# Kernel tuning notes

Measured on AMD Instinct MI355X. Metric: run time of the kernel, lower is better.

Reference implementation:

```python
import jax, jax.numpy as jnp
import numpy as np

EPS = 1e-8

def setup_inputs() -> dict:
    key = jax.random.key(0)
    k1, k2, k3 = jax.random.split(key, 3)
    B, D, H, W = 32, 96, 96, 96
    x = jax.random.normal(k1, (B, 1, D, H, W), dtype=jnp.float32)
    mask = jax.random.randint(k2, (1, 1, D, H, W), 0, 2, dtype=jnp.int32)
    weight = jax.random.normal(k3, (2, 1, D, H, W), dtype=jnp.float32) * 0.01
    bias = jnp.zeros((2,), dtype=jnp.float32)
    return {"x": x, "mask": mask, "weight": weight, "bias": bias}

def reference(x, mask, weight, bias):
    # effective positions: |x| > eps AND mask nonzero (values are NOT scaled by mask)
    gate = (jnp.abs(x) > EPS) & (mask != 0)          # (B,1,D,H,W) via broadcast
    xg = jnp.where(gate, x, jnp.zeros((), x.dtype))  # masked input
    # per-batch sparse dot products == dense masked contraction over all spatial dims
    out = jnp.einsum('bidhw,cidhw->bc', xg, weight) + bias  # (B, 2)
    # original reshapes to (B,2,1,1,1) then Flatten -> (B,2)
    return out
```

## Files before the change

kernel.cpp:

```cpp
#include <hip/hip_runtime.h>
#include <hip/hip_bf16.h>

#define EPS 1e-8f

constexpr int B_ = 32;
constexpr int N_ = 96 * 96 * 96;
constexpr int N4 = N_ / 4;
constexpr int TPB = 256;
constexpr int BPW = 8;
constexpr int NBLK = 1024;

__global__ __launch_bounds__(TPB) void partial_kernel(
    const float4* __restrict__ x,
    const int4*   __restrict__ mask,
    const float4* __restrict__ w,
    float*        __restrict__ partials)
{
    const int tid  = threadIdx.x;
    const int wave = tid >> 6;
    const int lane = tid & 63;
    const int b0   = wave * BPW;

    float acc[BPW][2];
#pragma unroll
    for (int bb = 0; bb < BPW; ++bb) { acc[bb][0] = 0.f; acc[bb][1] = 0.f; }

    const int stride = gridDim.x * 64;
    for (int i4 = blockIdx.x * 64 + lane; i4 < N4; i4 += stride) {
        const int4   mi = mask[i4];
        const float4 w0 = w[i4];
        const float4 w1 = w[N4 + i4];
        const float m0 = mi.x ? 1.f : 0.f;
        const float m1 = mi.y ? 1.f : 0.f;
        const float m2 = mi.z ? 1.f : 0.f;
        const float m3 = mi.w ? 1.f : 0.f;
        const float wm0x = w0.x * m0, wm0y = w0.y * m1, wm0z = w0.z * m2, wm0w = w0.w * m3;
        const float wm1x = w1.x * m0, wm1y = w1.y * m1, wm1z = w1.z * m2, wm1w = w1.w * m3;

#pragma unroll
        for (int bb = 0; bb < BPW; ++bb) {
            const float4 xv = x[(size_t)(b0 + bb) * N4 + i4];
            const float g0 = (fabsf(xv.x) > EPS) ? xv.x : 0.f;
            const float g1 = (fabsf(xv.y) > EPS) ? xv.y : 0.f;
            const float g2 = (fabsf(xv.z) > EPS) ? xv.z : 0.f;
            const float g3 = (fabsf(xv.w) > EPS) ? xv.w : 0.f;
            float a0 = acc[bb][0], a1 = acc[bb][1];
            a0 = fmaf(g0, wm0x, a0); a0 = fmaf(g1, wm0y, a0);
            a0 = fmaf(g2, wm0z, a0); a0 = fmaf(g3, wm0w, a0);
            a1 = fmaf(g0, wm1x, a1); a1 = fmaf(g1, wm1y, a1);
            a1 = fmaf(g2, wm1z, a1); a1 = fmaf(g3, wm1w, a1);
            acc[bb][0] = a0; acc[bb][1] = a1;
        }
    }

#pragma unroll
    for (int bb = 0; bb < BPW; ++bb) {
#pragma unroll
        for (int c = 0; c < 2; ++c) {
            float v = acc[bb][c];
            v += __shfl_xor(v, 32, 64);
            v += __shfl_xor(v, 16, 64);
            v += __shfl_xor(v,  8, 64);
            v += __shfl_xor(v,  4, 64);
            v += __shfl_xor(v,  2, 64);
            v += __shfl_xor(v,  1, 64);
            acc[bb][c] = v;
        }
    }

    __shared__ float lds[64];
    if (lane == 0) {
#pragma unroll
        for (int bb = 0; bb < BPW; ++bb) {
            lds[(b0 + bb) * 2 + 0] = acc[bb][0];
            lds[(b0 + bb) * 2 + 1] = acc[bb][1];
        }
    }
    __syncthreads();
    if (tid < 64) partials[(size_t)tid * gridDim.x + blockIdx.x] = lds[tid];
}

__global__ __launch_bounds__(256) void finalize_kernel(
    const float4* __restrict__ partials4,
    const float*  __restrict__ bias,
    float* __restrict__ out, int nblk4)
{
    const int j    = blockIdx.x;
    const int tid  = threadIdx.x;
    const int wave = tid >> 6;
    const int lane = tid & 63;

    float s = 0.f;
    for (int k = tid; k < nblk4; k += 256) {
        const float4 v = partials4[(size_t)j * nblk4 + k];
        s += (v.x + v.y) + (v.z + v.w);
    }
    s += __shfl_xor(s, 32, 64);
    s += __shfl_xor(s, 16, 64);
    s += __shfl_xor(s,  8, 64);
    s += __shfl_xor(s,  4, 64);
    s += __shfl_xor(s,  2, 64);
    s += __shfl_xor(s,  1, 64);

    __shared__ float red[4];
    if (lane == 0) red[wave] = s;
    __syncthreads();
    if (tid == 0)
        out[j] = (red[0] + red[1]) + (red[2] + red[3]) + bias[j & 1];
}

extern "C" void kernel_launch(void* const* d_in, const int* in_sizes, int n_in,
                              void* d_out, int out_size, void* d_ws, size_t ws_size,
                              hipStream_t stream) {
    const float4* x    = (const float4*)d_in[0];
    const int4*   mask = (const int4*)d_in[1];
    const float4* w    = (const float4*)d_in[2];
    const float*  bias = (const float*)d_in[3];
    float* out = (float*)d_out;
    float* partials = (float*)d_ws;

    int nblk = NBLK;
    const size_t need = (size_t)nblk * 64 * sizeof(float);
    if (ws_size < need) {
        nblk = (int)(ws_size / (64 * sizeof(float)));
        if (nblk < 4) nblk = 4;
        nblk &= ~3;
    }

    partial_kernel<<<nblk, TPB, 0, stream>>>(x, mask, w, partials);
    finalize_kernel<<<64, 256, 0, stream>>>((const float4*)partials, bias, out,
                                            nblk / 4);
}
```

Baseline: 29.02 us.

## Fully unroll grid-stride loop with double-buffered register prefetch

Adds a specialized kernel for the fixed 1024-block grid. The grid-stride loop (3–4 iterations per lane) is fully unrolled with two register stages, so the loads for the next iteration are issued before the current one is computed, giving more memory requests in flight. Each wave's lane 0 now writes partials straight to global memory instead of staging them through LDS behind a block barrier. This raises register pressure (two stages of 11 float4 each) and could reduce occupancy.

```diff
diff --git a/kernel.cpp b/kernel.cpp
--- a/kernel.cpp
+++ b/kernel.cpp
@@ -1,58 +1,59 @@
 #include <hip/hip_runtime.h>
-#include <hip/hip_bf16.h>
 
 #define EPS 1e-8f
 
-constexpr int B_ = 32;
-constexpr int N_ = 96 * 96 * 96;
-constexpr int N4 = N_ / 4;
-constexpr int TPB = 256;
-constexpr int BPW = 8;
+constexpr int N4   = 221184;
+constexpr int TPB  = 256;
+constexpr int BPW  = 8;
 constexpr int NBLK = 1024;
+constexpr int STR  = NBLK * 64;
 
-__global__ __launch_bounds__(TPB) void partial_kernel(
-    const float4* __restrict__ x,
-    const int4*   __restrict__ mask,
-    const float4* __restrict__ w,
-    float*        __restrict__ partials)
+struct Stage {
+    int4   mi;
+    float4 w0, w1;
+    float4 xv[BPW];
+};
+
+__device__ __forceinline__ void load_stage(Stage& s,
+        const float4* __restrict__ x, const int4* __restrict__ mask,
+        const float4* __restrict__ w, int i4, int b0)
 {
-    const int tid  = threadIdx.x;
-    const int wave = tid >> 6;
-    const int lane = tid & 63;
-    const int b0   = wave * BPW;
+    s.mi = mask[i4];
+    s.w0 = w[i4];
+    s.w1 = w[N4 + i4];
+#pragma unroll
+    for (int bb = 0; bb < BPW; ++bb)
+        s.xv[bb] = x[(size_t)(b0 + bb) * N4 + i4];
+}
 
-    float acc[BPW][2];
+__device__ __forceinline__ void compute_stage(const Stage& s, float (&acc)[BPW][2])
+{
+    const float m0 = s.mi.x ? 1.f : 0.f;
+    const float m1 = s.mi.y ? 1.f : 0.f;
+    const float m2 = s.mi.z ? 1.f : 0.f;
+    const float m3 = s.mi.w ? 1.f : 0.f;
+    const float wm0x = s.w0.x * m0, wm0y = s.w0.y * m1, wm0z = s.w0.z * m2, wm0w = s.w0.w * m3;
+    const float wm1x = s.w1.x * m0, wm1y = s.w1.y * m1, wm1z = s.w1.z * m2, wm1w = s.w1.w * m3;
 #pragma unroll
-    for (int bb = 0; bb < BPW; ++bb) { acc[bb][0] = 0.f; acc[bb][1] = 0.f; }
+    for (int bb = 0; bb < BPW; ++bb) {
+        const float4 xv = s.xv[bb];
+        const float g0 = (fabsf(xv.x) > EPS) ? xv.x : 0.f;
+        const float g1 = (fabsf(xv.y) > EPS) ? xv.y : 0.f;
+        const float g2 = (fabsf(xv.z) > EPS) ? xv.z : 0.f;
+        const float g3 = (fabsf(xv.w) > EPS) ? xv.w : 0.f;
+        float a0 = acc[bb][0], a1 = acc[bb][1];
+        a0 = fmaf(g0, wm0x, a0); a0 = fmaf(g1, wm0y, a0);
+        a0 = fmaf(g2, wm0z, a0); a0 = fmaf(g3, wm0w, a0);
+        a1 = fmaf(g0, wm1x, a1); a1 = fmaf(g1, wm1y, a1);
+        a1 = fmaf(g2, wm1z, a1); a1 = fmaf(g3, wm1w, a1);
+        acc[bb][0] = a0; acc[bb][1] = a1;
+    }
+}
 
-    const int stride = gridDim.x * 64;
-    for (int i4 = blockIdx.x * 64 + lane; i4 < N4; i4 += stride) {
-        const int4   mi = mask[i4];
-        const float4 w0 = w[i4];
-        const float4 w1 = w[N4 + i4];
-        const float m0 = mi.x ? 1.f : 0.f;
-        const float m1 = mi.y ? 1.f : 0.f;
-        const float m2 = mi.z ? 1.f : 0.f;
-        const float m3 = mi.w ? 1.f : 0.f;
-        const float wm0x = w0.x * m0, wm0y = w0.y * m1, wm0z = w0.z * m2, wm0w = w0.w * m3;
-        const float wm1x = w1.x * m0, wm1y = w1.y * m1, wm1z = w1.z * m2, wm1w = w1.w * m3;
-
-#pragma unroll
-        for (int bb = 0; bb < BPW; ++bb) {
-            const float4 xv = x[(size_t)(b0 + bb) * N4 + i4];
-            const float g0 = (fabsf(xv.x) > EPS) ? xv.x : 0.f;
-            const float g1 = (fabsf(xv.y) > EPS) ? xv.y : 0.f;
-            const float g2 = (fabsf(xv.z) > EPS) ? xv.z : 0.f;
-            const float g3 = (fabsf(xv.w) > EPS) ? xv.w : 0.f;
-            float a0 = acc[bb][0], a1 = acc[bb][1];
-            a0 = fmaf(g0, wm0x, a0); a0 = fmaf(g1, wm0y, a0);
-            a0 = fmaf(g2, wm0z, a0); a0 = fmaf(g3, wm0w, a0);
-            a1 = fmaf(g0, wm1x, a1); a1 = fmaf(g1, wm1y, a1);
-            a1 = fmaf(g2, wm1z, a1); a1 = fmaf(g3, wm1w, a1);
-            acc[bb][0] = a0; acc[bb][1] = a1;
-        }
-    }
-
+__device__ __forceinline__ void reduce_and_store(
+        float (&acc)[BPW][2], int wave, int lane, int b0, int bid, int nblk,
+        float* __restrict__ partials)
+{
 #pragma unroll
     for (int bb = 0; bb < BPW; ++bb) {
 #pragma unroll
@@ -67,22 +68,71 @@
             acc[bb][c] = v;
         }
     }
-
-    __shared__ float lds[64];
     if (lane == 0) {
 #pragma unroll
         for (int bb = 0; bb < BPW; ++bb) {
-            lds[(b0 + bb) * 2 + 0] = acc[bb][0];
-            lds[(b0 + bb) * 2 + 1] = acc[bb][1];
+            partials[(size_t)((b0 + bb) * 2 + 0) * nblk + bid] = acc[bb][0];
+            partials[(size_t)((b0 + bb) * 2 + 1) * nblk + bid] = acc[bb][1];
         }
     }
-    __syncthreads();
-    if (tid < 64) partials[(size_t)tid * gridDim.x + blockIdx.x] = lds[tid];
+}
+
+__global__ __launch_bounds__(TPB) void partial_static(
+    const float4* __restrict__ x, const int4* __restrict__ mask,
+    const float4* __restrict__ w, float* __restrict__ partials)
+{
+    const int tid  = threadIdx.x;
+    const int wave = tid >> 6;
+    const int lane = tid & 63;
+    const int b0   = wave * BPW;
+    const int bid  = blockIdx.x;
+    const int i4   = bid * 64 + lane;
+
+    float acc[BPW][2];
+#pragma unroll
+    for (int bb = 0; bb < BPW; ++bb) { acc[bb][0] = 0.f; acc[bb][1] = 0.f; }
+
+    Stage s0, s1;
+    load_stage(s0, x, mask, w, i4,       b0);
+    load_stage(s1, x, mask, w, i4 + STR, b0);
+    compute_stage(s0, acc);
+    load_stage(s0, x, mask, w, i4 + 2 * STR, b0);
+    compute_stage(s1, acc);
+    if (i4 + 3 * STR < N4) {
+        load_stage(s1, x, mask, w, i4 + 3 * STR, b0);
+        compute_stage(s0, acc);
+        compute_stage(s1, acc);
+    } else {
+        compute_stage(s0, acc);
+    }
+
+    reduce_and_store(acc, wave, lane, b0, bid, NBLK, partials);
+}
+
+__global__ __launch_bounds__(TPB) void partial_generic(
+    const float4* __restrict__ x, const int4* __restrict__ mask,
+    const float4* __restrict__ w, float* __restrict__ partials)
+{
+    const int tid  = threadIdx.x;
+    const int wave = tid >> 6;
+    const int lane = tid & 63;
+    const int b0   = wave * BPW;
+
+    float acc[BPW][2];
+#pragma unroll
+    for (int bb = 0; bb < BPW; ++bb) { acc[bb][0] = 0.f; acc[bb][1] = 0.f; }
+
+    const int stride = gridDim.x * 64;
+    for (int i4 = blockIdx.x * 64 + lane; i4 < N4; i4 += stride) {
+        Stage s;
+        load_stage(s, x, mask, w, i4, b0);
+        compute_stage(s, acc);
+    }
+    reduce_and_store(acc, wave, lane, b0, blockIdx.x, gridDim.x, partials);
 }
 
 __global__ __launch_bounds__(256) void finalize_kernel(
-    const float4* __restrict__ partials4,
-    const float*  __restrict__ bias,
+    const float4* __restrict__ partials4, const float* __restrict__ bias,
     float* __restrict__ out, int nblk4)
 {
     const int j    = blockIdx.x;
@@ -119,15 +169,16 @@
     float* out = (float*)d_out;
     float* partials = (float*)d_ws;
 
-    int nblk = NBLK;
-    const size_t need = (size_t)nblk * 64 * sizeof(float);
-    if (ws_size < need) {
-        nblk = (int)(ws_size / (64 * sizeof(float)));
+    if (ws_size >= (size_t)NBLK * 64 * sizeof(float)) {
+        partial_static<<<NBLK, TPB, 0, stream>>>(x, mask, w, partials);
+        finalize_kernel<<<64, 256, 0, stream>>>((const float4*)partials, bias,
+                                                out, NBLK / 4);
+    } else {
+        int nblk = (int)(ws_size / (64 * sizeof(float)));
         if (nblk < 4) nblk = 4;
         nblk &= ~3;
+        partial_generic<<<nblk, TPB, 0, stream>>>(x, mask, w, partials);
+        finalize_kernel<<<64, 256, 0, stream>>>((const float4*)partials, bias,
+                                                out, nblk / 4);
     }
-
-    partial_kernel<<<nblk, TPB, 0, stream>>>(x, mask, w, partials);
-    finalize_kernel<<<64, 256, 0, stream>>>((const float4*)partials, bias, out,
-                                            nblk / 4);
 }
```

After: 27.43 us. 5.5% less time.
